# Kernel optimization log

Hardware: AMD Instinct MI355X
Metric: run time of the kernel (lower is better)

## Reference

```python
import jax, jax.numpy as jnp
import numpy as np

T, B = 1024, 32
Q1, K1, V1 = 1024, 1024, 1024
Q2, K2, V2 = 1024, 1024, 1024
KW = 3  # kernel_width
EPS = 1e-6


def mask_softmax(x, mask):
    # softmax over dim 0 with multiplicative mask (exp(x-max)*mask / sum)
    e = jnp.exp(x - jnp.max(x, axis=0, keepdims=True))
    e = e * mask
    return e / jnp.sum(e, axis=0, keepdims=True)


def setup_inputs() -> dict:
    key = jax.random.key(0)
    ks = jax.random.split(key, 16)
    s = 0.02
    return {
        "q1": jax.random.normal(ks[0], (B, Q1), jnp.float32),
        "k1": jax.random.normal(ks[1], (T, B, K1), jnp.float32),
        "v1": jax.random.normal(ks[2], (T, B, V1), jnp.float32),
        "q2": jax.random.normal(ks[3], (B, Q2), jnp.float32),
        "k2": jax.random.normal(ks[4], (T, B, K2), jnp.float32),
        "v2": jax.random.normal(ks[5], (T, B, V2), jnp.float32),
        "k_mask": jnp.ones((T, B), jnp.float32),
        # Attention params: sa: Linear(q1_size -> align_size=K1); a1: Linear(K1 -> 1)
        "sa_w": jax.random.normal(ks[6], (K1, Q1), jnp.float32) * s,
        "sa_b": jnp.zeros((K1,), jnp.float32),
        "a1_w": jax.random.normal(ks[7], (1, K1), jnp.float32) * s,
        "a1_b": jnp.zeros((1,), jnp.float32),
        # AttCNN4Weight: q_to_kernel: Linear(q2_size -> k2_size*KW)
        "qk_w": jax.random.normal(ks[8], (K2 * KW, Q2), jnp.float32) * s,
        "qk_b": jnp.zeros((K2 * KW,), jnp.float32),
        # LayerNorm(v1_size)
        "ln_g": jnp.ones((V1,), jnp.float32),
        "ln_b": jnp.zeros((V1,), jnp.float32),
    }


def reference(q1, k1, v1, q2, k2, v2, k_mask,
              sa_w, sa_b, a1_w, a1_b, qk_w, qk_b, ln_g, ln_b):
    # ---- additive attention path ----
    # tanh(sa(q1)[None] + k1): [T, B, K1]
    t = jnp.tanh((q1 @ sa_w.T + sa_b)[None, :, :] + k1)
    a_1 = jnp.einsum('tba,a->tb', t, a1_w[0]) + a1_b[0]          # [T, B]
    e_1 = mask_softmax(a_1, k_mask)
    attend_1 = jnp.einsum('tb,tbd->bd', e_1, v1)                  # [B, V1]

    # ---- dynamic grouped-conv1d attention path ----
    kernel = (q2 @ qk_w.T + qk_b).reshape(B, K2, KW)              # per-example kernels
    pad = (KW - 1) // 2
    k2p = jnp.pad(k2, ((pad, pad), (0, 0), (0, 0)))               # [T+2p, B, K2]
    a_2 = jnp.zeros((T, B), k2.dtype)
    for w in range(KW):  # tiny fixed loop over kernel taps
        a_2 = a_2 + jnp.einsum('tbc,bc->tb', k2p[w:w + T], kernel[:, :, w])
    e_2 = mask_softmax(a_2, k_mask)
    attend_2 = jnp.einsum('tb,tbd->bd', e_2, v2)                  # [B, V2]

    # ---- combine: add + LayerNorm over feature dim ----
    x = attend_1 + attend_2
    mu = jnp.mean(x, axis=-1, keepdims=True)
    var = jnp.mean((x - mu) ** 2, axis=-1, keepdims=True)
    combined = (x - mu) * jax.lax.rsqrt(var + EPS) * ln_g + ln_b
    return combined
```

## Files before the change

kernel.cpp:

```cpp
#include <hip/hip_runtime.h>
#include <math.h>

#define T_DIM   1024
#define B_DIM   32
#define N_FEAT  1024
#define KW      3
#define NT      16
#define T_PER   (T_DIM / NT)
#define EPS     1e-6f

__global__ void __launch_bounds__(256) gemv_kernel(
    const float* __restrict__ x, const float* __restrict__ W,
    const float* __restrict__ bias, float* __restrict__ out,
    int N, int M) {
  int gtid = blockIdx.x * blockDim.x + threadIdx.x;
  int wid  = gtid >> 6;
  int lane = threadIdx.x & 63;
  int total = B_DIM * M;
  if (wid >= total) return;
  int b = wid / M, m = wid % M;
  const float4* xr = (const float4*)(x + (size_t)b * N);
  const float4* wr = (const float4*)(W + (size_t)m * N);
  float acc = 0.f;
  int n4 = N >> 2;
  for (int i = lane; i < n4; i += 64) {
    float4 xv = xr[i], wv = wr[i];
    acc += xv.x * wv.x + xv.y * wv.y + xv.z * wv.z + xv.w * wv.w;
  }
#pragma unroll
  for (int off = 32; off > 0; off >>= 1) acc += __shfl_down(acc, off, 64);
  if (lane == 0) out[wid] = acc + bias[m];
}

__global__ void __launch_bounds__(256) row_dots_kernel(
    const float* __restrict__ k1, const float* __restrict__ k2,
    const float* __restrict__ sa_q, const float* __restrict__ a1_w,
    const float* __restrict__ kern, const float* __restrict__ a1_b,
    float* __restrict__ a1_out, float* __restrict__ s_out) {
  int blk = blockIdx.x;
  int b   = blk % B_DIM;
  int tid = threadIdx.x;
  size_t row = (size_t)blk * N_FEAT + tid * 4;

  float4 k1v = *(const float4*)(k1 + row);
  float4 sqv = *(const float4*)(sa_q + (size_t)b * N_FEAT + tid * 4);
  float4 awv = *(const float4*)(a1_w + tid * 4);
  float p1 = tanhf(k1v.x + sqv.x) * awv.x
           + tanhf(k1v.y + sqv.y) * awv.y
           + tanhf(k1v.z + sqv.z) * awv.z
           + tanhf(k1v.w + sqv.w) * awv.w;

  float4 k2v = *(const float4*)(k2 + row);
  const float* kb = kern + (size_t)b * (N_FEAT * KW) + (size_t)tid * 4 * KW;
  float4 ka = *(const float4*)(kb);
  float4 kc = *(const float4*)(kb + 4);
  float4 kd = *(const float4*)(kb + 8);
  float kk[12] = {ka.x, ka.y, ka.z, ka.w, kc.x, kc.y, kc.z, kc.w,
                  kd.x, kd.y, kd.z, kd.w};
  float s0 = k2v.x * kk[0] + k2v.y * kk[3] + k2v.z * kk[6] + k2v.w * kk[9];
  float s1 = k2v.x * kk[1] + k2v.y * kk[4] + k2v.z * kk[7] + k2v.w * kk[10];
  float s2 = k2v.x * kk[2] + k2v.y * kk[5] + k2v.z * kk[8] + k2v.w * kk[11];

  float vals[4] = {p1, s0, s1, s2};
#pragma unroll
  for (int off = 32; off > 0; off >>= 1) {
#pragma unroll
    for (int j = 0; j < 4; j++) vals[j] += __shfl_down(vals[j], off, 64);
  }
  __shared__ float red[4][4];
  int wave = tid >> 6, lane = tid & 63;
  if (lane == 0) {
#pragma unroll
    for (int j = 0; j < 4; j++) red[wave][j] = vals[j];
  }
  __syncthreads();
  if (tid == 0) {
    float r0 = red[0][0] + red[1][0] + red[2][0] + red[3][0];
    float r1 = red[0][1] + red[1][1] + red[2][1] + red[3][1];
    float r2 = red[0][2] + red[1][2] + red[2][2] + red[3][2];
    float r3 = red[0][3] + red[1][3] + red[2][3] + red[3][3];
    a1_out[blk] = r0 + a1_b[0];
    s_out[(size_t)blk * 3 + 0] = r1;
    s_out[(size_t)blk * 3 + 1] = r2;
    s_out[(size_t)blk * 3 + 2] = r3;
  }
}

__device__ __forceinline__ float block_reduce_256(float v, bool is_max,
                                                  float* sm ) {
#pragma unroll
  for (int off = 32; off > 0; off >>= 1) {
    float o = __shfl_down(v, off, 64);
    v = is_max ? fmaxf(v, o) : v + o;
  }
  int wave = threadIdx.x >> 6;
  if ((threadIdx.x & 63) == 0) sm[wave] = v;
  __syncthreads();
  float r = is_max ? fmaxf(fmaxf(sm[0], sm[1]), fmaxf(sm[2], sm[3]))
                   : sm[0] + sm[1] + sm[2] + sm[3];
  __syncthreads();
  return r;
}

__global__ void __launch_bounds__(256) softmax_kernel(
    const float* __restrict__ a1, const float* __restrict__ s,
    const float* __restrict__ k_mask,
    float* __restrict__ e1, float* __restrict__ e2) {
  int b = blockIdx.x;
  int tid = threadIdx.x;
  __shared__ float sm[4];

  float x1[4], x2[4], mk[4];
#pragma unroll
  for (int k = 0; k < 4; k++) {
    int t = tid + k * 256;
    x1[k] = a1[(size_t)t * B_DIM + b];
    float sl = (t > 0)         ? s[((size_t)(t - 1) * B_DIM + b) * 3 + 0] : 0.f;
    float sc =                   s[((size_t)t       * B_DIM + b) * 3 + 1];
    float sr = (t < T_DIM - 1) ? s[((size_t)(t + 1) * B_DIM + b) * 3 + 2] : 0.f;
    x2[k] = sl + sc + sr;
    mk[k] = k_mask[(size_t)t * B_DIM + b];
  }
  float m1 = fmaxf(fmaxf(x1[0], x1[1]), fmaxf(x1[2], x1[3]));
  float m2 = fmaxf(fmaxf(x2[0], x2[1]), fmaxf(x2[2], x2[3]));
  m1 = block_reduce_256(m1, true, sm);
  m2 = block_reduce_256(m2, true, sm);

  float v1[4], v2[4], sum1 = 0.f, sum2 = 0.f;
#pragma unroll
  for (int k = 0; k < 4; k++) {
    v1[k] = expf(x1[k] - m1) * mk[k];
    v2[k] = expf(x2[k] - m2) * mk[k];
    sum1 += v1[k];
    sum2 += v2[k];
  }
  sum1 = block_reduce_256(sum1, false, sm);
  sum2 = block_reduce_256(sum2, false, sm);
  float i1 = 1.f / sum1, i2 = 1.f / sum2;
#pragma unroll
  for (int k = 0; k < 4; k++) {
    int t = tid + k * 256;
    e1[(size_t)t * B_DIM + b] = v1[k] * i1;
    e2[(size_t)t * B_DIM + b] = v2[k] * i2;
  }
}

__global__ void __launch_bounds__(256) weighted_v_kernel(
    const float* __restrict__ v1, const float* __restrict__ v2,
    const float* __restrict__ e1, const float* __restrict__ e2,
    float* __restrict__ partial) {
  int b  = blockIdx.x;
  int tc = blockIdx.y;
  int tid = threadIdx.x;
  __shared__ float se1[T_PER], se2[T_PER];
  if (tid < T_PER)
    se1[tid] = e1[(size_t)(tc * T_PER + tid) * B_DIM + b];
  else if (tid < 2 * T_PER)
    se2[tid - T_PER] = e2[(size_t)(tc * T_PER + (tid - T_PER)) * B_DIM + b];
  __syncthreads();

  float4 acc1 = {0.f, 0.f, 0.f, 0.f}, acc2 = {0.f, 0.f, 0.f, 0.f};
  size_t dofs = (size_t)tid * 4;
#pragma unroll 4
  for (int i = 0; i < T_PER; i++) {
    size_t row = ((size_t)(tc * T_PER + i) * B_DIM + b) * N_FEAT + dofs;
    float4 a = *(const float4*)(v1 + row);
    float4 c = *(const float4*)(v2 + row);
    float w1 = se1[i], w2 = se2[i];
    acc1.x += w1 * a.x; acc1.y += w1 * a.y; acc1.z += w1 * a.z; acc1.w += w1 * a.w;
    acc2.x += w2 * c.x; acc2.y += w2 * c.y; acc2.z += w2 * c.z; acc2.w += w2 * c.w;
  }
  size_t o1 = ((size_t)(0 * NT + tc) * B_DIM + b) * N_FEAT + dofs;
  size_t o2 = ((size_t)(1 * NT + tc) * B_DIM + b) * N_FEAT + dofs;
  *(float4*)(partial + o1) = acc1;
  *(float4*)(partial + o2) = acc2;
}

__device__ __forceinline__ float block_reduce_sum_1024(float v, float* sm) {
#pragma unroll
  for (int off = 32; off > 0; off >>= 1) v += __shfl_down(v, off, 64);
  int wave = threadIdx.x >> 6;
  if ((threadIdx.x & 63) == 0) sm[wave] = v;
  __syncthreads();
  float tot = 0.f;
#pragma unroll
  for (int i = 0; i < 16; i++) tot += sm[i];
  __syncthreads();
  return tot;
}

__global__ void __launch_bounds__(1024) ln_kernel(
    const float* __restrict__ partial, const float* __restrict__ ln_g,
    const float* __restrict__ ln_b, float* __restrict__ out) {
  int b = blockIdx.x;
  int d = threadIdx.x;
  __shared__ float sm[16];
  float x = 0.f;
#pragma unroll
  for (int j = 0; j < 2 * NT; j++)
    x += partial[((size_t)j * B_DIM + b) * N_FEAT + d];
  float ssum = block_reduce_sum_1024(x, sm);
  float mu = ssum * (1.f / N_FEAT);
  float dx = x - mu;
  float vsum = block_reduce_sum_1024(dx * dx, sm);
  float inv = rsqrtf(vsum * (1.f / N_FEAT) + EPS);
  out[(size_t)b * N_FEAT + d] = dx * inv * ln_g[d] + ln_b[d];
}

extern "C" void kernel_launch(void* const* d_in, const int* in_sizes, int n_in,
                              void* d_out, int out_size, void* d_ws, size_t ws_size,
                              hipStream_t stream) {
  const float* q1     = (const float*)d_in[0];
  const float* k1     = (const float*)d_in[1];
  const float* v1     = (const float*)d_in[2];
  const float* q2     = (const float*)d_in[3];
  const float* k2     = (const float*)d_in[4];
  const float* v2     = (const float*)d_in[5];
  const float* k_mask = (const float*)d_in[6];
  const float* sa_w   = (const float*)d_in[7];
  const float* sa_b   = (const float*)d_in[8];
  const float* a1_w   = (const float*)d_in[9];
  const float* a1_b   = (const float*)d_in[10];
  const float* qk_w   = (const float*)d_in[11];
  const float* qk_b   = (const float*)d_in[12];
  const float* ln_g   = (const float*)d_in[13];
  const float* ln_bp  = (const float*)d_in[14];
  float* out = (float*)d_out;
  float* ws  = (float*)d_ws;

  float* sa_q    = ws;
  float* kern    = sa_q + 32768;
  float* s       = kern + 98304;
  float* a1      = s + 98304;
  float* e1      = a1 + 32768;
  float* e2      = e1 + 32768;
  float* partial = e2 + 32768;

  gemv_kernel<<<dim3((B_DIM * 1024) >> 2), 256, 0, stream>>>(
      q1, sa_w, sa_b, sa_q, N_FEAT, 1024);
  gemv_kernel<<<dim3((B_DIM * 3072) >> 2), 256, 0, stream>>>(
      q2, qk_w, qk_b, kern, N_FEAT, 3072);
  row_dots_kernel<<<dim3(T_DIM * B_DIM), 256, 0, stream>>>(
      k1, k2, sa_q, a1_w, kern, a1_b, a1, s);
  softmax_kernel<<<dim3(B_DIM), 256, 0, stream>>>(a1, s, k_mask, e1, e2);
  weighted_v_kernel<<<dim3(B_DIM, NT), 256, 0, stream>>>(v1, v2, e1, e2, partial);
  ln_kernel<<<dim3(B_DIM), 1024, 0, stream>>>(partial, ln_g, ln_bp, out);
}
```

Measured before the change: 514.3 us.

## Fuse GEMVs, tile row-dots over time with shared-memory weights and prefetch

The two projection GEMVs are merged into one launch, and the conv kernel is stored transposed by tap. The row-dot kernel now has each block handle one batch element over 32 timesteps. Per-batch weights are staged once in shared memory and the next rows of k1/k2 are register-prefetched, instead of launching one block per (t,b) row with redundant weight loads. It also swaps tanhf/expf for fast approximations and doubles the time-split of the weighted-V stage with deeper unrolling. The fast tanh and exp may differ slightly in accuracy.

```diff
diff --git a/kernel.cpp b/kernel.cpp
--- a/kernel.cpp
+++ b/kernel.cpp
@@ -5,84 +5,135 @@
 #define B_DIM   32
 #define N_FEAT  1024
 #define KW      3
-#define NT      16
+#define NT      32
 #define T_PER   (T_DIM / NT)
+#define TT      32
 #define EPS     1e-6f
 
-__global__ void __launch_bounds__(256) gemv_kernel(
-    const float* __restrict__ x, const float* __restrict__ W,
-    const float* __restrict__ bias, float* __restrict__ out,
-    int N, int M) {
-  int gtid = blockIdx.x * blockDim.x + threadIdx.x;
-  int wid  = gtid >> 6;
+__device__ __forceinline__ float tanh_fast(float x) {
+  float ax = fminf(fabsf(x), 10.f);
+  float e  = __expf(ax + ax);
+  float r  = fmaf(-2.f, __builtin_amdgcn_rcpf(e + 1.f), 1.f);
+  return copysignf(r, x);
+}
+
+__global__ void __launch_bounds__(256) prep_kernel(
+    const float* __restrict__ q1, const float* __restrict__ sa_w,
+    const float* __restrict__ sa_b, const float* __restrict__ q2,
+    const float* __restrict__ qk_w, const float* __restrict__ qk_b,
+    float* __restrict__ sa_q, float* __restrict__ kern_t) {
+  int wid  = (blockIdx.x * 256 + threadIdx.x) >> 6;
   int lane = threadIdx.x & 63;
-  int total = B_DIM * M;
-  if (wid >= total) return;
-  int b = wid / M, m = wid % M;
-  const float4* xr = (const float4*)(x + (size_t)b * N);
-  const float4* wr = (const float4*)(W + (size_t)m * N);
+  int b = wid & (B_DIM - 1);
+  int m = wid >> 5;
+  const float4* xr;
+  const float4* wr;
+  if (m < 1024) {
+    xr = (const float4*)(q1 + (size_t)b * N_FEAT);
+    wr = (const float4*)(sa_w + (size_t)m * N_FEAT);
+  } else {
+    xr = (const float4*)(q2 + (size_t)b * N_FEAT);
+    wr = (const float4*)(qk_w + (size_t)(m - 1024) * N_FEAT);
+  }
   float acc = 0.f;
-  int n4 = N >> 2;
-  for (int i = lane; i < n4; i += 64) {
-    float4 xv = xr[i], wv = wr[i];
+#pragma unroll
+  for (int i = 0; i < 4; i++) {
+    float4 xv = xr[lane + 64 * i], wv = wr[lane + 64 * i];
     acc += xv.x * wv.x + xv.y * wv.y + xv.z * wv.z + xv.w * wv.w;
   }
 #pragma unroll
   for (int off = 32; off > 0; off >>= 1) acc += __shfl_down(acc, off, 64);
-  if (lane == 0) out[wid] = acc + bias[m];
-}
-
-__global__ void __launch_bounds__(256) row_dots_kernel(
+  if (lane == 0) {
+    if (m < 1024) {
+      sa_q[(size_t)b * N_FEAT + m] = acc + sa_b[m];
+    } else {
+      int mm = m - 1024;
+      int c = mm / 3, w = mm - 3 * c;
+      kern_t[(size_t)b * (N_FEAT * KW) + (size_t)w * N_FEAT + c] = acc + qk_b[mm];
+    }
+  }
+}
+
+__global__ void __launch_bounds__(256, 4) row_dots_kernel(
     const float* __restrict__ k1, const float* __restrict__ k2,
     const float* __restrict__ sa_q, const float* __restrict__ a1_w,
-    const float* __restrict__ kern, const float* __restrict__ a1_b,
+    const float* __restrict__ kern_t, const float* __restrict__ a1_b,
     float* __restrict__ a1_out, float* __restrict__ s_out) {
-  int blk = blockIdx.x;
-  int b   = blk % B_DIM;
-  int tid = threadIdx.x;
-  size_t row = (size_t)blk * N_FEAT + tid * 4;
-
-  float4 k1v = *(const float4*)(k1 + row);
-  float4 sqv = *(const float4*)(sa_q + (size_t)b * N_FEAT + tid * 4);
-  float4 awv = *(const float4*)(a1_w + tid * 4);
-  float p1 = tanhf(k1v.x + sqv.x) * awv.x
-           + tanhf(k1v.y + sqv.y) * awv.y
-           + tanhf(k1v.z + sqv.z) * awv.z
-           + tanhf(k1v.w + sqv.w) * awv.w;
-
-  float4 k2v = *(const float4*)(k2 + row);
-  const float* kb = kern + (size_t)b * (N_FEAT * KW) + (size_t)tid * 4 * KW;
-  float4 ka = *(const float4*)(kb);
-  float4 kc = *(const float4*)(kb + 4);
-  float4 kd = *(const float4*)(kb + 8);
-  float kk[12] = {ka.x, ka.y, ka.z, ka.w, kc.x, kc.y, kc.z, kc.w,
-                  kd.x, kd.y, kd.z, kd.w};
-  float s0 = k2v.x * kk[0] + k2v.y * kk[3] + k2v.z * kk[6] + k2v.w * kk[9];
-  float s1 = k2v.x * kk[1] + k2v.y * kk[4] + k2v.z * kk[7] + k2v.w * kk[10];
-  float s2 = k2v.x * kk[2] + k2v.y * kk[5] + k2v.z * kk[8] + k2v.w * kk[11];
-
-  float vals[4] = {p1, s0, s1, s2};
-#pragma unroll
-  for (int off = 32; off > 0; off >>= 1) {
-#pragma unroll
-    for (int j = 0; j < 4; j++) vals[j] += __shfl_down(vals[j], off, 64);
-  }
-  __shared__ float red[4][4];
-  int wave = tid >> 6, lane = tid & 63;
-  if (lane == 0) {
-#pragma unroll
-    for (int j = 0; j < 4; j++) red[wave][j] = vals[j];
-  }
-  __syncthreads();
-  if (tid == 0) {
-    float r0 = red[0][0] + red[1][0] + red[2][0] + red[3][0];
-    float r1 = red[0][1] + red[1][1] + red[2][1] + red[3][1];
-    float r2 = red[0][2] + red[1][2] + red[2][2] + red[3][2];
-    float r3 = red[0][3] + red[1][3] + red[2][3] + red[3][3];
-    a1_out[blk] = r0 + a1_b[0];
-    s_out[(size_t)blk * 3 + 0] = r1;
-    s_out[(size_t)blk * 3 + 1] = r2;
-    s_out[(size_t)blk * 3 + 2] = r3;
+  int b   = blockIdx.x;
+  int t0  = blockIdx.y * TT;
+  int tid = threadIdx.x, wave = tid >> 6, lane = tid & 63;
+
+  __shared__ float kw_s[KW][N_FEAT];
+  __shared__ float sq_s[N_FEAT];
+  __shared__ float aw_s[N_FEAT];
+  {
+    const float4* src = (const float4*)(kern_t + (size_t)b * (N_FEAT * KW));
+    float4* dst = (float4*)&kw_s[0][0];
+#pragma unroll
+    for (int i = 0; i < 3; i++) dst[tid + 256 * i] = src[tid + 256 * i];
+    ((float4*)sq_s)[tid] = ((const float4*)(sa_q + (size_t)b * N_FEAT))[tid];
+    ((float4*)aw_s)[tid] = ((const float4*)a1_w)[tid];
+  }
+  __syncthreads();
+  float a1bv = a1_b[0];
+
+  float4 c1[4], c2[4];
+  {
+    size_t rb = ((size_t)(t0 + wave) * B_DIM + b) * N_FEAT;
+#pragma unroll
+    for (int ch = 0; ch < 4; ch++) {
+      c1[ch] = *(const float4*)(k1 + rb + ch * 256 + lane * 4);
+      c2[ch] = *(const float4*)(k2 + rb + ch * 256 + lane * 4);
+    }
+  }
+  for (int i = 0; i < TT / 4; i++) {
+    int t = t0 + 4 * i + wave;
+    float4 n1[4], n2[4];
+    if (i + 1 < TT / 4) {
+      size_t nb = ((size_t)(t + 4) * B_DIM + b) * N_FEAT;
+#pragma unroll
+      for (int ch = 0; ch < 4; ch++) {
+        n1[ch] = *(const float4*)(k1 + nb + ch * 256 + lane * 4);
+        n2[ch] = *(const float4*)(k2 + nb + ch * 256 + lane * 4);
+      }
+    } else {
+#pragma unroll
+      for (int ch = 0; ch < 4; ch++) { n1[ch] = c1[ch]; n2[ch] = c2[ch]; }
+    }
+    float p1 = 0.f, s0 = 0.f, s1 = 0.f, s2 = 0.f;
+#pragma unroll
+    for (int ch = 0; ch < 4; ch++) {
+      int f = ch * 256 + lane * 4;
+      float4 A  = c1[ch], Bv = c2[ch];
+      float4 sq = *(const float4*)&sq_s[f];
+      float4 aw = *(const float4*)&aw_s[f];
+      p1 += tanh_fast(A.x + sq.x) * aw.x;
+      p1 += tanh_fast(A.y + sq.y) * aw.y;
+      p1 += tanh_fast(A.z + sq.z) * aw.z;
+      p1 += tanh_fast(A.w + sq.w) * aw.w;
+      float4 w0 = *(const float4*)&kw_s[0][f];
+      float4 w1 = *(const float4*)&kw_s[1][f];
+      float4 w2 = *(const float4*)&kw_s[2][f];
+      s0 += Bv.x * w0.x + Bv.y * w0.y + Bv.z * w0.z + Bv.w * w0.w;
+      s1 += Bv.x * w1.x + Bv.y * w1.y + Bv.z * w1.z + Bv.w * w1.w;
+      s2 += Bv.x * w2.x + Bv.y * w2.y + Bv.z * w2.z + Bv.w * w2.w;
+    }
+#pragma unroll
+    for (int off = 32; off > 0; off >>= 1) {
+      p1 += __shfl_xor(p1, off, 64);
+      s0 += __shfl_xor(s0, off, 64);
+      s1 += __shfl_xor(s1, off, 64);
+      s2 += __shfl_xor(s2, off, 64);
+    }
+    if (lane == 0) {
+      size_t o = (size_t)t * B_DIM + b;
+      a1_out[o] = p1 + a1bv;
+      s_out[o * 3 + 0] = s0;
+      s_out[o * 3 + 1] = s1;
+      s_out[o * 3 + 2] = s2;
+    }
+#pragma unroll
+    for (int ch = 0; ch < 4; ch++) { c1[ch] = n1[ch]; c2[ch] = n2[ch]; }
   }
 }
 
@@ -129,8 +180,8 @@
   float v1[4], v2[4], sum1 = 0.f, sum2 = 0.f;
 #pragma unroll
   for (int k = 0; k < 4; k++) {
-    v1[k] = expf(x1[k] - m1) * mk[k];
-    v2[k] = expf(x2[k] - m2) * mk[k];
+    v1[k] = __expf(x1[k] - m1) * mk[k];
+    v2[k] = __expf(x2[k] - m2) * mk[k];
     sum1 += v1[k];
     sum2 += v2[k];
   }
@@ -161,14 +212,16 @@
 
   float4 acc1 = {0.f, 0.f, 0.f, 0.f}, acc2 = {0.f, 0.f, 0.f, 0.f};
   size_t dofs = (size_t)tid * 4;
-#pragma unroll 4
+#pragma unroll 8
   for (int i = 0; i < T_PER; i++) {
     size_t row = ((size_t)(tc * T_PER + i) * B_DIM + b) * N_FEAT + dofs;
     float4 a = *(const float4*)(v1 + row);
     float4 c = *(const float4*)(v2 + row);
     float w1 = se1[i], w2 = se2[i];
-    acc1.x += w1 * a.x; acc1.y += w1 * a.y; acc1.z += w1 * a.z; acc1.w += w1 * a.w;
-    acc2.x += w2 * c.x; acc2.y += w2 * c.y; acc2.z += w2 * c.z; acc2.w += w2 * c.w;
+    acc1.x = fmaf(w1, a.x, acc1.x); acc1.y = fmaf(w1, a.y, acc1.y);
+    acc1.z = fmaf(w1, a.z, acc1.z); acc1.w = fmaf(w1, a.w, acc1.w);
+    acc2.x = fmaf(w2, c.x, acc2.x); acc2.y = fmaf(w2, c.y, acc2.y);
+    acc2.z = fmaf(w2, c.z, acc2.z); acc2.w = fmaf(w2, c.w, acc2.w);
   }
   size_t o1 = ((size_t)(0 * NT + tc) * B_DIM + b) * N_FEAT + dofs;
   size_t o2 = ((size_t)(1 * NT + tc) * B_DIM + b) * N_FEAT + dofs;
@@ -227,21 +280,20 @@
   const float* ln_bp  = (const float*)d_in[14];
   float* out = (float*)d_out;
   float* ws  = (float*)d_ws;
+  (void)k_mask;
 
   float* sa_q    = ws;
-  float* kern    = sa_q + 32768;
-  float* s       = kern + 98304;
+  float* kern_t  = sa_q + 32768;
+  float* s       = kern_t + 98304;
   float* a1      = s + 98304;
   float* e1      = a1 + 32768;
   float* e2      = e1 + 32768;
   float* partial = e2 + 32768;
 
-  gemv_kernel<<<dim3((B_DIM * 1024) >> 2), 256, 0, stream>>>(
-      q1, sa_w, sa_b, sa_q, N_FEAT, 1024);
-  gemv_kernel<<<dim3((B_DIM * 3072) >> 2), 256, 0, stream>>>(
-      q2, qk_w, qk_b, kern, N_FEAT, 3072);
-  row_dots_kernel<<<dim3(T_DIM * B_DIM), 256, 0, stream>>>(
-      k1, k2, sa_q, a1_w, kern, a1_b, a1, s);
+  prep_kernel<<<dim3((4096 * B_DIM) / 4), 256, 0, stream>>>(
+      q1, sa_w, sa_b, q2, qk_w, qk_b, sa_q, kern_t);
+  row_dots_kernel<<<dim3(B_DIM, T_DIM / TT), 256, 0, stream>>>(
+      k1, k2, sa_q, a1_w, kern_t, a1_b, a1, s);
   softmax_kernel<<<dim3(B_DIM), 256, 0, stream>>>(a1, s, k_mask, e1, e2);
   weighted_v_kernel<<<dim3(B_DIM, NT), 256, 0, stream>>>(v1, v2, e1, e2, partial);
   ln_kernel<<<dim3(B_DIM), 1024, 0, stream>>>(partial, ln_g, ln_bp, out);
```

Result: slower. 554.8 us (+7.9%).
